# Kernel tuning notes

Measured on AMD Instinct MI355X. Metric: run time of the kernel, lower is better.

## Reference

```python
import jax, jax.numpy as jnp
import numpy as np

P = 16; D = 1024; NH = 16; MAG = 4
B = 2; V = 4; H = 256; W = 512
DEPTH = 6; NE = 2; NM = 3   # dense-early, sparse-middle, rest dense-late
L = (H // P) * (W // P)    # 512 tokens
KEEP = L // 4              # keep_ratio = 0.25 -> 128 hard tokens
HD = D // NH
SCALE = HD ** -0.5


def setup_inputs() -> dict:
    key = jax.random.key(0)
    ks = iter(jax.random.split(key, 64))
    def rn(shape, s=0.02):
        return jax.random.normal(next(ks), shape, jnp.float32) * s
    inp = {}
    inp['x'] = jax.random.normal(next(ks), (B, V, H, W), jnp.float32)
    # select_hard_tokens: per-row randperm(L)[:K], sorted -> deterministic input
    rng = np.random.default_rng(0)
    hi = np.stack([np.sort(rng.permutation(L)[:KEEP]) for _ in range(B)]).astype(np.int32)
    inp['hard_idx'] = jnp.asarray(hi)
    inp['patch_w'] = rn((V, P * P, D)); inp['patch_b'] = jnp.zeros((V, D), jnp.float32)
    inp['var_embed'] = rn((V, D)); inp['var_query'] = rn((D,))
    inp['agg_wq'] = rn((D, D)); inp['agg_wk'] = rn((D, D))
    inp['agg_wv'] = rn((D, D)); inp['agg_wo'] = rn((D, D))
    inp['agg_bo'] = jnp.zeros((D,), jnp.float32)
    inp['pos_embed'] = rn((L, D), 1.0)
    inp['ln1_w'] = jnp.ones((DEPTH, D), jnp.float32); inp['ln1_b'] = jnp.zeros((DEPTH, D), jnp.float32)
    inp['qkv_w'] = rn((DEPTH, D, 3 * D)); inp['qkv_b'] = jnp.zeros((DEPTH, 3 * D), jnp.float32)
    inp['aproj_w'] = rn((DEPTH, D, D)); inp['aproj_b'] = jnp.zeros((DEPTH, D), jnp.float32)
    inp['ln2_w'] = jnp.ones((DEPTH, D), jnp.float32); inp['ln2_b'] = jnp.zeros((DEPTH, D), jnp.float32)
    inp['fc1_w'] = rn((DEPTH, D, 4 * D)); inp['fc1_b'] = jnp.zeros((DEPTH, 4 * D), jnp.float32)
    inp['fc2_w'] = rn((DEPTH, 4 * D, D)); inp['fc2_b'] = jnp.zeros((DEPTH, D), jnp.float32)
    inp['norm_w'] = jnp.ones((D,), jnp.float32); inp['norm_b'] = jnp.zeros((D,), jnp.float32)
    inp['head_w'] = rn((2, D, D)); inp['head_b'] = jnp.zeros((2, D), jnp.float32)
    inp['head_out_w'] = rn((D, (MAG * P) ** 2)); inp['head_out_b'] = jnp.zeros(((MAG * P) ** 2,), jnp.float32)
    inp['p2c1_w'] = rn((4 * MAG * MAG, V, 3, 3)); inp['p2c1_b'] = jnp.zeros((4 * MAG * MAG,), jnp.float32)
    inp['p2c2_w'] = rn((1, 4, 3, 3)); inp['p2c2_b'] = jnp.zeros((1,), jnp.float32)
    inp['cout_w'] = rn((1, 1, 3, 3)); inp['cout_b'] = jnp.zeros((1,), jnp.float32)
    return inp


def _ln(x, g, b):
    m = jnp.mean(x, -1, keepdims=True)
    v = jnp.mean((x - m) ** 2, -1, keepdims=True)
    return (x - m) * jax.lax.rsqrt(v + 1e-5) * g + b


def _conv3x3(x, w, b):
    y = jax.lax.conv_general_dilated(x, w, (1, 1), 'SAME',
                                     dimension_numbers=('NCHW', 'OIHW', 'NCHW'))
    return y + b[None, :, None, None]


def _pixel_shuffle(x, r):
    b, c, h, w = x.shape
    c2 = c // (r * r)
    return x.reshape(b, c2, r, r, h, w).transpose(0, 1, 4, 2, 5, 3).reshape(b, c2, h * r, w * r)


def _block_step(c, p):
    l1w, l1b, qw, qb, pw, pb, l2w, l2b, f1w, f1b, f2w, f2b = p
    bsz, n, _ = c.shape
    hn = _ln(c, l1w, l1b)
    qkv = (hn @ qw + qb).reshape(bsz, n, 3, NH, HD).transpose(2, 0, 3, 1, 4)  # 3,b,h,n,d
    qh, kh, vh = qkv[0], qkv[1], qkv[2]
    att = jax.nn.softmax(jnp.einsum('bhqd,bhkd->bhqk', qh, kh) * SCALE, axis=-1)
    o = jnp.einsum('bhqk,bhkd->bhqd', att, vh).transpose(0, 2, 1, 3).reshape(bsz, n, D)
    c = c + o @ pw + pb
    hn2 = _ln(c, l2w, l2b)
    c = c + jax.nn.gelu(hn2 @ f1w + f1b, approximate=False) @ f2w + f2b
    return c, None


def reference(x, hard_idx, patch_w, patch_b, var_embed, var_query,
              agg_wq, agg_wk, agg_wv, agg_wo, agg_bo, pos_embed,
              ln1_w, ln1_b, qkv_w, qkv_b, aproj_w, aproj_b,
              ln2_w, ln2_b, fc1_w, fc1_b, fc2_w, fc2_b,
              norm_w, norm_b, head_w, head_b, head_out_w, head_out_b,
              p2c1_w, p2c1_b, p2c2_w, p2c2_b, cout_w, cout_b):
    b_, v_, h_img, w_img = x.shape
    hh, ww = h_img // P, w_img // P
    ltok = hh * ww
    # per-variable patch embedding (PatchEmbed with in_chans=1)
    xp = x.reshape(b_, v_, hh, P, ww, P).transpose(0, 1, 2, 4, 3, 5).reshape(b_, v_, ltok, P * P)
    tok = jnp.einsum('bvle,ved->bvld', xp, patch_w) + patch_b[None, :, None, :]
    tok = tok + var_embed[None, :, None, :]
    # aggregate_variables: cross-attention query over V per token
    xf = tok.transpose(0, 2, 1, 3).reshape(b_ * ltok, v_, D)
    q = (var_query @ agg_wq).reshape(NH, HD)
    k = (xf @ agg_wk).reshape(-1, v_, NH, HD)
    vv = (xf @ agg_wv).reshape(-1, v_, NH, HD)
    a = jax.nn.softmax(jnp.einsum('hd,nvhd->nhv', q, k) * SCALE, axis=-1)
    agg = jnp.einsum('nhv,nvhd->nhd', a, vv).reshape(-1, D) @ agg_wo + agg_bo
    xt = agg.reshape(b_, ltok, D) + pos_embed[None]
    stacked = (ln1_w, ln1_b, qkv_w, qkv_b, aproj_w, aproj_b,
               ln2_w, ln2_b, fc1_w, fc1_b, fc2_w, fc2_b)
    def run(c, s, e):
        c, _ = jax.lax.scan(_block_step, c, tuple(ar[s:e] for ar in stacked))
        return c
    # dense early blocks (all tokens)
    xt = run(xt, 0, NE)
    # gather hard tokens -> sparse middle blocks; easy tokens skip via identity
    hard = jnp.take_along_axis(xt, hard_idx[:, :, None].astype(jnp.int32), axis=1)
    hard = run(hard, NE, NE + NM)
    brow = jnp.arange(b_)[:, None]
    xt = xt.at[brow, hard_idx].set(hard)  # merge_tokens (easy = identity)
    # dense late blocks
    xt = run(xt, NE + NM, DEPTH)
    xt = _ln(xt, norm_w, norm_b)
    # decoder head
    for i in range(head_w.shape[0]):
        xt = jax.nn.gelu(xt @ head_w[i] + head_b[i], approximate=False)
    pred = xt @ head_out_w + head_out_b  # (B, L, (MAG*P)^2)
    # unpatchify with scaling=MAG
    h2, w2 = h_img * MAG // P, w_img * MAG // P
    y = pred.reshape(b_, h2, w2, P, P, 1)
    y = jnp.einsum('nhwpqc->nchpwq', y).reshape(b_, 1, h2 * P, w2 * P)
    # residual path2 on raw input channels (out_var_index = all 4 channels here)
    r = jax.nn.gelu(_conv3x3(x, p2c1_w, p2c1_b), approximate=False)
    r = _pixel_shuffle(r, MAG)
    r = _conv3x3(r, p2c2_w, p2c2_b)
    return _conv3x3(y + r, cout_w, cout_b)
```

## Files before the change

kernel.cpp:

```cpp
#include <hip/hip_runtime.h>
#include <math.h>


#define UNIT 1048576L

typedef __attribute__((ext_vector_type(8))) short short8;
typedef __attribute__((ext_vector_type(4))) float f32x4;

#define GLDS(gp, lp) __builtin_amdgcn_global_load_lds( \
    (const __attribute__((address_space(1))) void*)(gp), \
    (__attribute__((address_space(3))) void*)(lp), 16, 0, 0)

__device__ __forceinline__ float gelu_f(float v){
  return 0.5f*v*(1.0f + erff(v*0.70710678118654752440f));
}

__device__ __forceinline__ unsigned short f2bf(float f){
  union { float f; unsigned u; } a; a.f = f;
  unsigned r = a.u + 0x7fffu + ((a.u >> 16) & 1u);
  return (unsigned short)(r >> 16);
}
__device__ __forceinline__ float bf2f(unsigned short u){
  union { unsigned u; float f; } a; a.u = (unsigned)u << 16;
  return a.f;
}

struct WJobs {
  const float* W[4];
  unsigned short* T[4];
  int K[4], N[4];
  int start[4];
};

__global__ __launch_bounds__(256)
void wtrans_multi(WJobs J)
{
  __shared__ float tile[32][33];
  int bx = blockIdx.x;
  int j = 0;
  #pragma unroll
  for (int i = 1; i < 4; ++i) if (bx >= J.start[i]) j = i;
  int local = bx - J.start[j];
  int K = J.K[j], N = J.N[j];
  int nx = N >> 5, tpb = (K >> 5) * nx;
  int bz = local / tpb, rem = local % tpb;
  int k0 = (rem / nx) * 32, n0 = (rem % nx) * 32;
  const float* Wp = J.W[j] + (long)bz * K * N;
  unsigned short* Wo = J.T[j] + (long)bz * K * N;
  int tx = threadIdx.x & 31, ty = threadIdx.x >> 5;
  #pragma unroll
  for (int i = 0; i < 4; ++i)
    tile[ty*4+i][tx] = Wp[(long)(k0 + ty*4 + i)*N + n0 + tx];
  __syncthreads();
  #pragma unroll
  for (int i = 0; i < 4; ++i){
    int n = ty*4 + i;
    Wo[(long)(n0 + n)*K + k0 + tx] = f2bf(tile[tx][n]);
  }
}

template<int TM>
__global__ __launch_bounds__(256)
void gemm_bt(const unsigned short* __restrict__ A, const unsigned short* __restrict__ Wt,
             const float* __restrict__ bias, const float* __restrict__ res,
// ... 81 lines not shown
  #pragma unroll
  for (int i = 0; i < 4; ++i){
    int rbase = row0 + wm + i*16 + kg*4;
    #pragma unroll
    for (int j = 0; j < NJ; ++j){
      int c = col0 + wn + j*16 + ln;
      float bv = bptr ? bptr[c] : 0.f;
      #pragma unroll
      for (int rr2 = 0; rr2 < 4; ++rr2){
        int rrow = rbase + rr2;
        float v = acc[i][j][rr2] + bv;
        if (rptr) v += rptr[(long)rrow*ldc + c];
        if (act == 1) v = gelu_f(v);
        if (Cf) Cf[(long)rrow*ldc + c] = v;
        if (Cb) Cb[(long)rrow*ldc + c] = f2bf(v);
      }
    }
  }
}

__global__ __launch_bounds__(256)
void reduce_ep(const float* __restrict__ Cp, int splits, int nbat, long MN, int N,
               const float* __restrict__ bias, const float* __restrict__ res, long sRes,
               float* __restrict__ Cf, unsigned short* __restrict__ Cb, long sC, int act)
{
  long e4 = (long)blockIdx.x*256 + threadIdx.x;
  if (e4 >= (long)nbat*MN/4) return;
  long e = e4 * 4;
  int b = (int)(e / MN); long r = e % MN; int col = (int)(r % N);
  float4 s = *(const float4*)&Cp[(long)b*MN + r];
  for (int sp = 1; sp < splits; ++sp){
    float4 p = *(const float4*)&Cp[((long)sp*nbat + b)*MN + r];
    s.x += p.x; s.y += p.y; s.z += p.z; s.w += p.w;
  }
  if (bias){
    float4 bv = *(const float4*)&bias[col];
    s.x += bv.x; s.y += bv.y; s.z += bv.z; s.w += bv.w;
  }
  if (res){
    float4 rv = *(const float4*)&res[(long)b*sRes + r];
    s.x += rv.x; s.y += rv.y; s.z += rv.z; s.w += rv.w;
  }
  if (act == 1){
    s.x = gelu_f(s.x); s.y = gelu_f(s.y); s.z = gelu_f(s.z); s.w = gelu_f(s.w);
  }
  if (Cf) *(float4*)&Cf[(long)b*sC + r] = s;
  if (Cb){
    unsigned q0 = (unsigned)f2bf(s.x) | ((unsigned)f2bf(s.y) << 16);
    unsigned q1 = (unsigned)f2bf(s.z) | ((unsigned)f2bf(s.w) << 16);
    uint2 pk = {q0, q1};
    *(uint2*)&Cb[(long)b*sC + r] = pk;
  }
}

__global__ __launch_bounds__(256)
void ln_bf(const float* __restrict__ x, const float* __restrict__ g,
           const float* __restrict__ b, unsigned short* __restrict__ y)
{
  long r = blockIdx.x;
  int t = threadIdx.x;
  float4 v = ((const float4*)(x + r*1024))[t];
  float s  = v.x + v.y + v.z + v.w;
  float ss = v.x*v.x + v.y*v.y + v.z*v.z + v.w*v.w;
  #pragma unroll
  for (int o = 32; o; o >>= 1){ s += __shfl_xor(s, o); ss += __shfl_xor(ss, o); }
  __shared__ float sa[4], sb[4];
  int w = t >> 6, lane = t & 63;
  if (!lane){ sa[w] = s; sb[w] = ss; }
  __syncthreads();
  s  = sa[0] + sa[1] + sa[2] + sa[3];
  ss = sb[0] + sb[1] + sb[2] + sb[3];
  float mean = s * (1.0f/1024.0f);
  float var  = ss * (1.0f/1024.0f) - mean*mean;
  float rstd = rsqrtf(var + 1e-5f);
  float4 gv = ((const float4*)g)[t];
  float4 bv = ((const float4*)b)[t];
  float ox = (v.x-mean)*rstd*gv.x + bv.x;
  float oy = (v.y-mean)*rstd*gv.y + bv.y;
  float oz = (v.z-mean)*rstd*gv.z + bv.z;
  float ow = (v.w-mean)*rstd*gv.w + bv.w;
  unsigned q0 = (unsigned)f2bf(ox) | ((unsigned)f2bf(oy) << 16);
  unsigned q1 = (unsigned)f2bf(oz) | ((unsigned)f2bf(ow) << 16);
  uint2 pk = {q0, q1};
  *(uint2*)&y[r*1024 + t*4] = pk;
}

__global__ void xp_extract(const float* __restrict__ x, unsigned short* __restrict__ xp)
{
  int idx = blockIdx.x * 256 + threadIdx.x;
  int e4 = idx & 63;
  int lt = (idx >> 6) & 511;
  int zz = idx >> 15;
  int e  = e4 << 2;
  int py = e >> 4, px0 = e & 15;
  int hy = lt >> 5, wx = lt & 31;
  float4 v = *(const float4*)&x[((long)zz*256 + hy*16 + py)*512 + wx*16 + px0];
  unsigned q0 = (unsigned)f2bf(v.x) | ((unsigned)f2bf(v.y) << 16);
  unsigned q1 = (unsigned)f2bf(v.z) | ((unsigned)f2bf(v.w) << 16);
  uint2 pk = {q0, q1};
  ((uint2*)xp)[idx] = pk;
}

__global__ void pb2_combine(const float* __restrict__ pb, const float* __restrict__ ve,
                            float* __restrict__ out)
{
  int i = blockIdx.x * 256 + threadIdx.x;
  out[i] = pb[i] + ve[i];
}

__global__ void qproj(const float* __restrict__ vq, const float* __restrict__ wq,
                      float* __restrict__ q)
{
  int n = blockIdx.x * 64 + threadIdx.x;
  float s = 0.f;
  for (int k = 0; k < 1024; ++k) s += vq[k] * wq[(long)k*1024 + n];
  q[n] = s;
}

__global__ void wk_fold(const float* __restrict__ wk, const float* __restrict__ qv,
                        float* __restrict__ wt)
{
  int i = blockIdx.x * 256 + threadIdx.x;
  int h = i & 15, D = i >> 4;
  const float* wr = wk + (long)D*1024 + h*64;
  const float* qr = qv + h*64;
  float s = 0.f;
  #pragma unroll
  for (int d = 0; d < 64; ++d) s += wr[d]*qr[d];
  wt[h*1024 + D] = s;
}

__global__ __launch_bounds__(64)
void agg_attn2(const unsigned short* __restrict__ tok, const float* __restrict__ vb,
               const float* __restrict__ wt, unsigned short* __restrict__ out)
{
  int l = blockIdx.x, h = blockIdx.y, b = blockIdx.z, t = threadIdx.x;
  const float* wh = wt + h*1024;
  float sc[4];
  #pragma unroll
  for (int v = 0; v < 4; ++v){
    const unsigned short* tr = tok + ((((long)b*4 + v)*512 + l) << 10);
    float s = 0.f;
    #pragma unroll
    for (int j = 0; j < 16; ++j){
      int D = t + j*64;
      s += bf2f(tr[D]) * wh[D];
    }
    #pragma unroll
    for (int o = 32; o; o >>= 1) s += __shfl_xor(s, o);
    sc[v] = s * 0.125f;
  }
  float m = fmaxf(fmaxf(sc[0], sc[1]), fmaxf(sc[2], sc[3]));
  float e0 = __expf(sc[0]-m), e1 = __expf(sc[1]-m), e2 = __expf(sc[2]-m), e3 = __expf(sc[3]-m);
  float inv = 1.0f / (e0 + e1 + e2 + e3);
  long base = (((long)b*4)*512 + l)*1024 + h*64 + t;
  float o = e0*vb[base] + e1*vb[base + 512*1024] + e2*vb[base + 2*512*1024] + e3*vb[base + 3*512*1024];
  out[(((long)b*512 + l) << 10) + h*64 + t] = f2bf(o * inv);
}

__global__ __launch_bounds__(256)
void attn_mfma(const float* __restrict__ qkv, unsigned short* __restrict__ out, int N)
{
  int h = blockIdx.y, b = blockIdx.z;
  int row0 = blockIdx.x * 32;
  int t = threadIdx.x;
  int wave = t >> 6, lane = t & 63;
  int ln = lane & 15, kg = lane >> 4;
  int mtile = wave & 1, khalf = wave >> 1;
  const float* base = qkv + (long)b * N * 3072;

  __shared__ __align__(16) unsigned short Ks[128*72];
  __shared__ __align__(16) unsigned short Vt[64*136];
  __shared__ __align__(16) unsigned short Pw[4][16*72];
  __shared__ float Obuf[4][16][68];
  __shared__ float Mbuf[4][16], Lbuf[4][16];

  short8 qf[2];
  {
    const float* qp = base + (long)(row0 + mtile*16 + ln)*3072 + h*64;
    #pragma unroll
    for (int s = 0; s < 2; ++s){
      float4 a = *(const float4*)(qp + s*32 + kg*8);
      float4 c = *(const float4*)(qp + s*32 + kg*8 + 4);
      short8 q;
      q[0] = (short)f2bf(a.x*0.125f); q[1] = (short)f2bf(a.y*0.125f);
      q[2] = (short)f2bf(a.z*0.125f); q[3] = (short)f2bf(a.w*0.125f);
      q[4] = (short)f2bf(c.x*0.125f); q[5] = (short)f2bf(c.y*0.125f);
      q[6] = (short)f2bf(c.z*0.125f); q[7] = (short)f2bf(c.w*0.125f);
      qf[s] = q;
    }
  }

  f32x4 z = {0.f, 0.f, 0.f, 0.f};
  f32x4 O[4] = {z, z, z, z};
  float mrow[4] = {-1e30f, -1e30f, -1e30f, -1e30f};
  float lrow[4] = {0.f, 0.f, 0.f, 0.f};
  unsigned short* pw = &Pw[wave][0];

  for (int j0 = 0; j0 < N; j0 += 128){
    #pragma unroll
    for (int it = 0; it < 2; ++it){
      int key = (t >> 2) + it*64;
      int dg = (t & 3) * 16;
      const float* kp = base + (long)(j0 + key)*3072 + 1024 + h*64 + dg;
      float4 k0 = *(const float4*)kp,     k1 = *(const float4*)(kp+4);
      float4 k2 = *(const float4*)(kp+8), k3 = *(const float4*)(kp+12);
      unsigned short* kd = &Ks[key*72 + dg];
      uint2 p0 = { (unsigned)f2bf(k0.x) | ((unsigned)f2bf(k0.y)<<16),
                   (unsigned)f2bf(k0.z) | ((unsigned)f2bf(k0.w)<<16) };
      uint2 p1 = { (unsigned)f2bf(k1.x) | ((unsigned)f2bf(k1.y)<<16),
                   (unsigned)f2bf(k1.z) | ((unsigned)f2bf(k1.w)<<16) };
      uint2 p2 = { (unsigned)f2bf(k2.x) | ((unsigned)f2bf(k2.y)<<16),
                   (unsigned)f2bf(k2.z) | ((unsigned)f2bf(k2.w)<<16) };
      uint2 p3 = { (unsigned)f2bf(k3.x) | ((unsigned)f2bf(k3.y)<<16),
                   (unsigned)f2bf(k3.z) | ((unsigned)f2bf(k3.w)<<16) };
      *(uint2*)&kd[0]  = p0; *(uint2*)&kd[4]  = p1;
      *(uint2*)&kd[8]  = p2; *(uint2*)&kd[12] = p3;
      const float* vp = base + (long)(j0 + key)*3072 + 2048 + h*64 + dg;
      float4 v0 = *(const float4*)vp,     v1 = *(const float4*)(vp+4);
      float4 v2 = *(const float4*)(vp+8), v3 = *(const float4*)(vp+12);
      float vv[16];
      vv[0]=v0.x; vv[1]=v0.y; vv[2]=v0.z; vv[3]=v0.w;
      vv[4]=v1.x; vv[5]=v1.y; vv[6]=v1.z; vv[7]=v1.w;
      vv[8]=v2.x; vv[9]=v2.y; vv[10]=v2.z; vv[11]=v2.w;
      vv[12]=v3.x; vv[13]=v3.y; vv[14]=v3.z; vv[15]=v3.w;
      #pragma unroll
      for (int i = 0; i < 16; ++i) Vt[(dg+i)*136 + key] = f2bf(vv[i]);
    }
    __syncthreads();

    f32x4 acc[4] = {z, z, z, z};
    const unsigned short* kbase = &Ks[(khalf*64)*72];
    #pragma unroll
    for (int s = 0; s < 2; ++s){
      #pragma unroll
      for (int nt = 0; nt < 4; ++nt){
        short8 bf = *(const short8*)&kbase[(nt*16 + ln)*72 + s*32 + kg*8];
        acc[nt] = __builtin_amdgcn_mfma_f32_16x16x32_bf16(qf[s], bf, acc[nt], 0, 0, 0);
      }
    }

    #pragma unroll
    for (int r = 0; r < 4; ++r){
      float mt = fmaxf(fmaxf(acc[0][r], acc[1][r]), fmaxf(acc[2][r], acc[3][r]));
      #pragma unroll
      for (int o = 1; o < 16; o <<= 1) mt = fmaxf(mt, __shfl_xor(mt, o));
      float m_new = fmaxf(mrow[r], mt);
      float alpha = __expf(mrow[r] - m_new);
      float ps = 0.f;
      #pragma unroll
// ... 39 lines not shown
  float ma = Mbuf[wa][lr],  mb2 = Mbuf[wa+2][lr];
  float la = Lbuf[wa][lr],  lb  = Lbuf[wa+2][lr];
  float mm = fmaxf(ma, mb2);
  float ea = __expf(ma - mm), eb = __expf(mb2 - mm);
  float linv = 1.0f / (la*ea + lb*eb);
  ea *= linv; eb *= linv;
  float4 a0 = *(const float4*)&Obuf[wa][lr][d0];
  float4 a1 = *(const float4*)&Obuf[wa][lr][d0+4];
  float4 b0 = *(const float4*)&Obuf[wa+2][lr][d0];
  float4 b1 = *(const float4*)&Obuf[wa+2][lr][d0+4];
  float o0 = a0.x*ea + b0.x*eb, o1 = a0.y*ea + b0.y*eb;
  float o2 = a0.z*ea + b0.z*eb, o3 = a0.w*ea + b0.w*eb;
  float o4 = a1.x*ea + b1.x*eb, o5 = a1.y*ea + b1.y*eb;
  float o6 = a1.z*ea + b1.z*eb, o7 = a1.w*ea + b1.w*eb;
  unsigned q0 = (unsigned)f2bf(o0) | ((unsigned)f2bf(o1) << 16);
  unsigned q1 = (unsigned)f2bf(o2) | ((unsigned)f2bf(o3) << 16);
  unsigned q2 = (unsigned)f2bf(o4) | ((unsigned)f2bf(o5) << 16);
  unsigned q3 = (unsigned)f2bf(o6) | ((unsigned)f2bf(o7) << 16);
  uint4 pk = {q0, q1, q2, q3};
  *(uint4*)&out[((long)(b*N + row0 + row))*1024 + h*64 + d0] = pk;
}

__global__ __launch_bounds__(256)
void gather_rows(const float* __restrict__ src, const int* __restrict__ idx,
                 float* __restrict__ dst)
{
  int r = blockIdx.x;
  int b = r >> 7, i = r & 127;
  int s = idx[b*128 + i];
  ((float4*)(dst + (long)r*1024))[threadIdx.x] =
      ((const float4*)(src + ((long)b*512 + s)*1024))[threadIdx.x];
}
__global__ __launch_bounds__(256)
void scatter_rows(const float* __restrict__ src, const int* __restrict__ idx,
                  float* __restrict__ dst)
{
  int r = blockIdx.x;
  int b = r >> 7, i = r & 127;
  int s = idx[b*128 + i];
  ((float4*)(dst + ((long)b*512 + s)*1024))[threadIdx.x] =
      ((const float4*)(src + (long)r*1024))[threadIdx.x];
}

__global__ __launch_bounds__(256)
void conv1_v4(const float* __restrict__ x, const float* __restrict__ w,
              const float* __restrict__ bi, unsigned short* __restrict__ out)
{
  __shared__ unsigned short obuf[256*68];
  int t = threadIdx.x;
  int id = blockIdx.x*256 + t;
  int px = id & 511, py = (id >> 9) & 255, bb = id >> 17;
  float in[4][9];
  #pragma unroll
  for (int ci = 0; ci < 4; ++ci){
    const float* xc = x + ((long)(bb*4 + ci)*256)*512;
    #pragma unroll
    for (int ky = 0; ky < 3; ++ky){
      int yy = py + ky - 1;
      #pragma unroll
      for (int kx = 0; kx < 3; ++kx){
        int xx = px + kx - 1;
        bool ok = ((unsigned)yy < 256u) && ((unsigned)xx < 512u);
        in[ci][ky*3+kx] = ok ? xc[yy*512 + xx] : 0.f;
      }
    }
  }
  unsigned short* orow = &obuf[t*68];
// ... 120 lines not shown
  }
}

static inline void gemm_go(hipStream_t st, int TM, const unsigned short* A,
                           const unsigned short* Wt,
                           const float* bias, const float* res, float* Cf, unsigned short* Cb,
                           float* Cp, int splits,
                           int M, int N, int K, int batches,
                           long sA, long sW, long sBias, long sRes, long sC,
                           int wmod, int act)
{
  dim3 g(N/128, M/TM, batches*splits);
  long MN = (long)M*N;
  if (TM == 128)
    gemm_bt<128><<<g, 256, 0, st>>>(A, Wt, bias, res, Cf, Cb, Cp, MN, splits,
                                    M, N, K, N, sA, sW, sBias, sRes, sC, wmod, act);
  else
    gemm_bt<64><<<g, 256, 0, st>>>(A, Wt, bias, res, Cf, Cb, Cp, MN, splits,
                                   M, N, K, N, sA, sW, sBias, sRes, sC, wmod, act);
}

static inline void reduce_go(hipStream_t st, const float* Cp, int splits, int nbat,
                             long MN, int N, const float* bias, const float* res, long sRes,
                             float* Cf, unsigned short* Cb, long sC, int act)
{
  long total4 = (long)nbat*MN/4;
  reduce_ep<<<(int)((total4 + 255)/256), 256, 0, st>>>(Cp, splits, nbat, MN, N,
                                                       bias, res, sRes, Cf, Cb, sC, act);
}

static inline void wmulti_go(hipStream_t st, int njobs,
                             const float* W0, unsigned short* T0, int K0, int N0, int nb0,
                             const float* W1, unsigned short* T1, int K1, int N1, int nb1,
                             const float* W2, unsigned short* T2, int K2, int N2, int nb2,
                             const float* W3, unsigned short* T3, int K3, int N3, int nb3)
{
  WJobs J;
  const float* Ws[4] = {W0, W1, W2, W3};
  unsigned short* Ts[4] = {T0, T1, T2, T3};
  int Ks[4] = {K0, K1, K2, K3}, Ns[4] = {N0, N1, N2, N3}, nbs[4] = {nb0, nb1, nb2, nb3};
  int acc = 0;
  for (int i = 0; i < 4; ++i){
    if (i < njobs){
      J.W[i] = Ws[i]; J.T[i] = Ts[i]; J.K[i] = Ks[i]; J.N[i] = Ns[i];
      J.start[i] = acc;
      acc += nbs[i] * (Ks[i] >> 5) * (Ns[i] >> 5);
    } else {
      J.W[i] = Ws[0]; J.T[i] = Ts[0]; J.K[i] = 32; J.N[i] = 32;
      J.start[i] = 0x7fffffff;
    }
  }
  wtrans_multi<<<acc, 256, 0, st>>>(J);
}

extern "C" void kernel_launch(void* const* d_in, const int* in_sizes, int n_in,
                              void* d_out, int out_size, void* d_ws, size_t ws_size,
                              hipStream_t stream)
{
  const float* x         = (const float*)d_in[0];
  const int*   hard_idx  = (const int*)  d_in[1];
  const float* patch_w   = (const float*)d_in[2];
  const float* patch_b   = (const float*)d_in[3];
  const float* var_embed = (const float*)d_in[4];
  const float* var_query = (const float*)d_in[5];
  const float* agg_wq    = (const float*)d_in[6];
  const float* agg_wk    = (const float*)d_in[7];
  const float* agg_wv    = (const float*)d_in[8];
  const float* agg_wo    = (const float*)d_in[9];
  const float* agg_bo    = (const float*)d_in[10];
  const float* pos_embed = (const float*)d_in[11];
  const float* ln1_w     = (const float*)d_in[12];
  const float* ln1_b     = (const float*)d_in[13];
  const float* qkv_w     = (const float*)d_in[14];
  const float* qkv_b     = (const float*)d_in[15];
  const float* aproj_w   = (const float*)d_in[16];
  const float* aproj_b   = (const float*)d_in[17];
  const float* ln2_w     = (const float*)d_in[18];
  const float* ln2_b     = (const float*)d_in[19];
  const float* fc1_w     = (const float*)d_in[20];
  const float* fc1_b     = (const float*)d_in[21];
  const float* fc2_w     = (const float*)d_in[22];
  const float* fc2_b     = (const float*)d_in[23];
  const float* norm_w    = (const float*)d_in[24];
  const float* norm_b    = (const float*)d_in[25];
  const float* head_w    = (const float*)d_in[26];
  const float* head_b    = (const float*)d_in[27];
  const float* head_out_w= (const float*)d_in[28];
  const float* head_out_b= (const float*)d_in[29];
  const float* p2c1_w    = (const float*)d_in[30];
  const float* p2c1_b    = (const float*)d_in[31];
  const float* p2c2_w    = (const float*)d_in[32];
  const float* p2c2_b    = (const float*)d_in[33];
  const float* cout_w    = (const float*)d_in[34];
  const float* cout_b    = (const float*)d_in[35];

  float* ws = (float*)d_ws;
  float* xt   = ws;
  float* r2   = ws + 1*UNIT;
  float* qkvb = ws + 5*UNIT;
  float* pred = ws + 8*UNIT;
  unsigned short* rbig = (unsigned short*)(ws + 8*UNIT);
  float* vb   = ws + 12*UNIT;
  float* Cp   = ws + 12*UNIT;
  unsigned short* b16 = (unsigned short*)(ws + 16*UNIT);
  unsigned short* hn_bf    = b16;
  unsigned short* ao_bf    = b16 + 1*UNIT;
  unsigned short* ff_bf    = b16 + 2*UNIT;
  unsigned short* xp_bf    = b16 + 6*UNIT;
  unsigned short* tok_bf   = b16 + 7*UNIT;
  unsigned short* aggin_bf = b16 + 11*UNIT;
  unsigned short* wt_a     = b16 + 12*UNIT;
  float* tail = ws + 28*UNIT;
  float* pb2  = tail;
  float* qv   = tail + 4096;
  float* wtl  = tail + 5120;
  float* hbuf = tail + 21504;

  conv1_v4<<<1024, 256, 0, stream>>>(x, p2c1_w, p2c1_b, rbig);
  conv2_v3<<<dim3(32, 64, 2), 256, 0, stream>>>(rbig, p2c2_w, p2c2_b, r2);

  unsigned short* wt_patch = wt_a;
  unsigned short* wt_wv    = wt_a + 1*UNIT;
  unsigned short* wt_wo    = wt_a + 2*UNIT;
  pb2_combine<<<16, 256, 0, stream>>>(patch_b, var_embed, pb2);
  xp_extract<<<1024, 256, 0, stream>>>(x, xp_bf);
  qproj<<<16, 64, 0, stream>>>(var_query, agg_wq, qv);
  wk_fold<<<64, 256, 0, stream>>>(agg_wk, qv, wtl);
  wmulti_go(stream, 3,
            patch_w, wt_patch, 256, 1024, 4,
            agg_wv,  wt_wv,   1024, 1024, 1,
            agg_wo,  wt_wo,   1024, 1024, 1,
            nullptr, nullptr, 0, 0, 0);
  gemm_go(stream, 128, xp_bf, wt_patch, pb2, nullptr, nullptr, tok_bf, nullptr, 1,
          512, 1024, 256, 8, 512L*256, 256L*1024, 1024, 0, 512L*1024, 4, 0);
  gemm_go(stream, 128, tok_bf, wt_wv, nullptr, nullptr, vb, nullptr, nullptr, 1,
          512, 1024, 1024, 8, 512L*1024, 0, 0, 0, 512L*1024, 1, 0);
  agg_attn2<<<dim3(512, 16, 2), 64, 0, stream>>>(tok_bf, vb, wtl, aggin_bf);
  gemm_go(stream, 64, aggin_bf, wt_wo, nullptr, nullptr, nullptr, nullptr, Cp, 2,
          512, 1024, 1024, 2, 512L*1024, 0, 0, 0, 512L*1024, 1, 0);
  reduce_go(stream, Cp, 2, 2, 512L*1024, 1024, agg_bo, pos_embed, 0, xt, nullptr,
            512L*1024, 0);

  unsigned short* wt_qkv   = wt_a;
  unsigned short* wt_aproj = wt_a + 3*UNIT;
  unsigned short* wt_fc1   = wt_a + 4*UNIT;
  unsigned short* wt_fc2   = wt_a + 8*UNIT;

  auto run_block = [&](float* cur, int Nt, int d){
    int rows = 2 * Nt;
    bool dense = (rows >= 1024);
    int TMbig = dense ? 128 : 64;
    long MNq = (long)rows*3072, MNa = (long)rows*1024, MNf = (long)rows*4096;
    wmulti_go(stream, 4,
              qkv_w   + (long)d*1024*3072, wt_qkv,   1024, 3072, 1,
              aproj_w + (long)d*1024*1024, wt_aproj, 1024, 1024, 1,
              fc1_w   + (long)d*1024*4096, wt_fc1,   1024, 4096, 1,
              fc2_w   + (long)d*4096*1024, wt_fc2,   4096, 1024, 1);
    ln_bf<<<rows, 256, 0, stream>>>(cur, ln1_w + d*1024, ln1_b + d*1024, hn_bf);
    gemm_go(stream, TMbig, hn_bf, wt_qkv, qkv_b + d*3072, nullptr, qkvb, nullptr, nullptr, 1,
            rows, 3072, 1024, 1, 0, 0, 0, 0, 0, 1, 0);
    attn_mfma<<<dim3(Nt/32, 16, 2), 256, 0, stream>>>(qkvb, ao_bf, Nt);
    {
      int sk = dense ? 4 : 8;
      gemm_go(stream, TMbig, ao_bf, wt_aproj, nullptr, nullptr, nullptr, nullptr, Cp, sk,
              rows, 1024, 1024, 1, 0, 0, 0, 0, 0, 1, 0);
      reduce_go(stream, Cp, sk, 1, MNa, 1024, aproj_b + d*1024, cur, MNa, cur, nullptr, MNa, 0);
    }
    ln_bf<<<rows, 256, 0, stream>>>(cur, ln2_w + d*1024, ln2_b + d*1024, hn_bf);
    if (dense){
      gemm_go(stream, 128, hn_bf, wt_fc1, fc1_b + d*4096, nullptr, nullptr, ff_bf, nullptr, 1,
              rows, 4096, 1024, 1, 0, 0, 0, 0, 0, 1, 1);
    } else {
      gemm_go(stream, 64, hn_bf, wt_fc1, nullptr, nullptr, nullptr, nullptr, Cp, 2,
              rows, 4096, 1024, 1, 0, 0, 0, 0, 0, 1, 1);
      reduce_go(stream, Cp, 2, 1, MNf, 4096, fc1_b + d*4096, nullptr, 0, nullptr, ff_bf, MNf, 1);
    }
    {
      int sk = dense ? 4 : 8;
      gemm_go(stream, TMbig, ff_bf, wt_fc2, nullptr, nullptr, nullptr, nullptr, Cp, sk,
              rows, 1024, 4096, 1, 0, 0, 0, 0, 0, 1, 0);
      reduce_go(stream, Cp, sk, 1, MNa, 1024, fc2_b + d*1024, cur, MNa, cur, nullptr, MNa, 0);
    }
  };

  run_block(xt, 512, 0);
  run_block(xt, 512, 1);
  gather_rows<<<256, 256, 0, stream>>>(xt, hard_idx, hbuf);
  run_block(hbuf, 128, 2);
  run_block(hbuf, 128, 3);
  run_block(hbuf, 128, 4);
  scatter_rows<<<256, 256, 0, stream>>>(hbuf, hard_idx, xt);
  run_block(xt, 512, 5);

  unsigned short* wt_h1 = wt_a;
  unsigned short* wt_h2 = wt_a + 1*UNIT;
  unsigned short* wt_ho = wt_a + 2*UNIT;
  wmulti_go(stream, 3,
            head_w,              wt_h1, 1024, 1024, 1,
            head_w + 1024L*1024, wt_h2, 1024, 1024, 1,
            head_out_w,          wt_ho, 1024, 4096, 1,
            nullptr, nullptr, 0, 0, 0);
  ln_bf<<<1024, 256, 0, stream>>>(xt, norm_w, norm_b, hn_bf);
  gemm_go(stream, 64, hn_bf, wt_h1, nullptr, nullptr, nullptr, nullptr, Cp, 2,
          1024, 1024, 1024, 1, 0, 0, 0, 0, 0, 1, 1);
  reduce_go(stream, Cp, 2, 1, 1024L*1024, 1024, head_b, nullptr, 0, nullptr, ao_bf,
            1024L*1024, 1);
  gemm_go(stream, 64, ao_bf, wt_h2, nullptr, nullptr, nullptr, nullptr, Cp, 2,
          1024, 1024, 1024, 1, 0, 0, 0, 0, 0, 1, 1);
  reduce_go(stream, Cp, 2, 1, 1024L*1024, 1024, head_b + 1024, nullptr, 0, nullptr, hn_bf,
            1024L*1024, 1);
  gemm_go(stream, 128, hn_bf, wt_ho, head_out_b, nullptr, pred, nullptr, nullptr, 1,
          1024, 4096, 1024, 1, 0, 0, 0, 0, 0, 1, 0);

  cout_fused<<<dim3(32, 64, 2), 256, 0, stream>>>(pred, r2, cout_w, cout_b, (float*)d_out);
}
```

Baseline: 1.373 ms.

## Fuse residual reduce with LayerNorm, batch weight transposes, keep QKV in bf16

All weight transposes for every layer and the head now run in one upfront launch instead of one launch per block. The split-K reduce is fused with the next LayerNorm (reduce_ln), the gather is fused with LN, and the scatter is folded into the last sparse block's reduce epilogue via an index table. The QKV output and the aggregation V are stored as bf16, so the attention kernels read half the bytes and skip conversion. The QKV GEMM now uses split-K plus a reduce, which adds a partial-buffer round trip. The workspace footprint grows to hold all transposed weights.

```diff
diff --git a/kernel.cpp b/kernel.cpp
--- a/kernel.cpp
+++ b/kernel.cpp
@@ -26,10 +26,10 @@
 }
 
 struct WJobs {
-  const float* W[4];
-  unsigned short* T[4];
-  int K[4], N[4];
-  int start[4];
+  const float* W[10];
+  unsigned short* T[10];
+  int K[10], N[10];
+  int start[10];
 };
 
 __global__ __launch_bounds__(256)
@@ -39,7 +39,7 @@
   int bx = blockIdx.x;
   int j = 0;
   #pragma unroll
-  for (int i = 1; i < 4; ++i) if (bx >= J.start[i]) j = i;
+  for (int i = 1; i < 10; ++i) if (bx >= J.start[i]) j = i;
   int local = bx - J.start[j];
   int K = J.K[j], N = J.N[j];
   int nx = N >> 5, tpb = (K >> 5) * nx;
@@ -167,7 +167,8 @@
 __global__ __launch_bounds__(256)
 void reduce_ep(const float* __restrict__ Cp, int splits, int nbat, long MN, int N,
                const float* __restrict__ bias, const float* __restrict__ res, long sRes,
-               float* __restrict__ Cf, unsigned short* __restrict__ Cb, long sC, int act)
+               float* __restrict__ Cf, unsigned short* __restrict__ Cb, long sC, int act,
+               const int* __restrict__ sidx)
 {
   long e4 = (long)blockIdx.x*256 + threadIdx.x;
   if (e4 >= (long)nbat*MN/4) return;
@@ -189,13 +190,70 @@
   if (act == 1){
     s.x = gelu_f(s.x); s.y = gelu_f(s.y); s.z = gelu_f(s.z); s.w = gelu_f(s.w);
   }
-  if (Cf) *(float4*)&Cf[(long)b*sC + r] = s;
+  if (Cf){
+    if (sidx){
+      int rw = (int)(r >> 10); int bt = rw >> 7, ii = rw & 127;
+      long orow = (long)bt*512 + sidx[bt*128 + ii];
+      *(float4*)&Cf[orow*1024 + (r & 1023)] = s;
+    } else {
+      *(float4*)&Cf[(long)b*sC + r] = s;
+    }
+  }
   if (Cb){
     unsigned q0 = (unsigned)f2bf(s.x) | ((unsigned)f2bf(s.y) << 16);
     unsigned q1 = (unsigned)f2bf(s.z) | ((unsigned)f2bf(s.w) << 16);
     uint2 pk = {q0, q1};
     *(uint2*)&Cb[(long)b*sC + r] = pk;
   }
+}
+
+__global__ __launch_bounds__(256)
+void reduce_ln(const float* __restrict__ Cp, int splits, int nbat, long MN,
+               const float* __restrict__ bias,
+               const float* __restrict__ res, long sRes,
+               float* __restrict__ cur,
+               const float* __restrict__ g, const float* __restrict__ b,
+               unsigned short* __restrict__ hn)
+{
+  int row = blockIdx.x;
+  int t = threadIdx.x;
+  int rpb = (int)(MN >> 10);
+  int bb = row / rpb;
+  long r = (long)(row - bb*rpb)*1024 + t*4;
+  float4 s = *(const float4*)&Cp[(long)bb*MN + r];
+  for (int sp = 1; sp < splits; ++sp){
+    float4 p = *(const float4*)&Cp[((long)sp*nbat + bb)*MN + r];
+    s.x += p.x; s.y += p.y; s.z += p.z; s.w += p.w;
+  }
+  int col = t*4;
+  float4 bv = *(const float4*)&bias[col];
+  s.x += bv.x; s.y += bv.y; s.z += bv.z; s.w += bv.w;
+  float4 rv = *(const float4*)&res[(long)bb*sRes + r];
+  s.x += rv.x; s.y += rv.y; s.z += rv.z; s.w += rv.w;
+  *(float4*)&cur[(long)row*1024 + col] = s;
+  float sm = s.x + s.y + s.z + s.w;
+  float ss = s.x*s.x + s.y*s.y + s.z*s.z + s.w*s.w;
+  #pragma unroll
+  for (int o = 32; o; o >>= 1){ sm += __shfl_xor(sm, o); ss += __shfl_xor(ss, o); }
+  __shared__ float sa[4], sb[4];
+  int w = t >> 6, lane = t & 63;
+  if (!lane){ sa[w] = sm; sb[w] = ss; }
+  __syncthreads();
+  sm = sa[0] + sa[1] + sa[2] + sa[3];
+  ss = sb[0] + sb[1] + sb[2] + sb[3];
+  float mean = sm * (1.0f/1024.0f);
+  float var  = ss * (1.0f/1024.0f) - mean*mean;
+  float rstd = rsqrtf(var + 1e-5f);
+  float4 gv = ((const float4*)g)[t];
+  float4 bv2 = ((const float4*)b)[t];
+  float ox = (s.x-mean)*rstd*gv.x + bv2.x;
+  float oy = (s.y-mean)*rstd*gv.y + bv2.y;
+  float oz = (s.z-mean)*rstd*gv.z + bv2.z;
+  float ow = (s.w-mean)*rstd*gv.w + bv2.w;
+  unsigned q0 = (unsigned)f2bf(ox) | ((unsigned)f2bf(oy) << 16);
+  unsigned q1 = (unsigned)f2bf(oz) | ((unsigned)f2bf(ow) << 16);
+  uint2 pk = {q0, q1};
+  *(uint2*)&hn[(long)row*1024 + col] = pk;
 }
 
 __global__ __launch_bounds__(256)
@@ -230,6 +288,41 @@
   *(uint2*)&y[r*1024 + t*4] = pk;
 }
 
+__global__ __launch_bounds__(256)
+void gather_ln(const float* __restrict__ src, const int* __restrict__ idx,
+               float* __restrict__ dst, const float* __restrict__ g,
+               const float* __restrict__ b, unsigned short* __restrict__ hn)
+{
+  int r = blockIdx.x, t = threadIdx.x;
+  int bb = r >> 7, i = r & 127;
+  int s0 = idx[bb*128 + i];
+  float4 v = ((const float4*)(src + ((long)bb*512 + s0)*1024))[t];
+  ((float4*)(dst + (long)r*1024))[t] = v;
+  float s  = v.x + v.y + v.z + v.w;
+  float ss = v.x*v.x + v.y*v.y + v.z*v.z + v.w*v.w;
+  #pragma unroll
+  for (int o = 32; o; o >>= 1){ s += __shfl_xor(s, o); ss += __shfl_xor(ss, o); }
+  __shared__ float sa[4], sb[4];
+  int w = t >> 6, lane = t & 63;
+  if (!lane){ sa[w] = s; sb[w] = ss; }
+  __syncthreads();
+  s  = sa[0] + sa[1] + sa[2] + sa[3];
+  ss = sb[0] + sb[1] + sb[2] + sb[3];
+  float mean = s * (1.0f/1024.0f);
+  float var  = ss * (1.0f/1024.0f) - mean*mean;
+  float rstd = rsqrtf(var + 1e-5f);
+  float4 gv = ((const float4*)g)[t];
+  float4 bv = ((const float4*)b)[t];
+  float ox = (v.x-mean)*rstd*gv.x + bv.x;
+  float oy = (v.y-mean)*rstd*gv.y + bv.y;
+  float oz = (v.z-mean)*rstd*gv.z + bv.z;
+  float ow = (v.w-mean)*rstd*gv.w + bv.w;
+  unsigned q0 = (unsigned)f2bf(ox) | ((unsigned)f2bf(oy) << 16);
+  unsigned q1 = (unsigned)f2bf(oz) | ((unsigned)f2bf(ow) << 16);
+  uint2 pk = {q0, q1};
+  *(uint2*)&hn[(long)r*1024 + t*4] = pk;
+}
+
 __global__ void xp_extract(const float* __restrict__ x, unsigned short* __restrict__ xp)
 {
   int idx = blockIdx.x * 256 + threadIdx.x;
@@ -276,7 +369,7 @@
 }
 
 __global__ __launch_bounds__(64)
-void agg_attn2(const unsigned short* __restrict__ tok, const float* __restrict__ vb,
+void agg_attn2(const unsigned short* __restrict__ tok, const unsigned short* __restrict__ vb,
                const float* __restrict__ wt, unsigned short* __restrict__ out)
 {
   int l = blockIdx.x, h = blockIdx.y, b = blockIdx.z, t = threadIdx.x;
@@ -299,12 +392,14 @@
   float e0 = __expf(sc[0]-m), e1 = __expf(sc[1]-m), e2 = __expf(sc[2]-m), e3 = __expf(sc[3]-m);
   float inv = 1.0f / (e0 + e1 + e2 + e3);
   long base = (((long)b*4)*512 + l)*1024 + h*64 + t;
-  float o = e0*vb[base] + e1*vb[base + 512*1024] + e2*vb[base + 2*512*1024] + e3*vb[base + 3*512*1024];
+  float o = e0*bf2f(vb[base]) + e1*bf2f(vb[base + 512*1024])
+          + e2*bf2f(vb[base + 2*512*1024]) + e3*bf2f(vb[base + 3*512*1024]);
   out[(((long)b*512 + l) << 10) + h*64 + t] = f2bf(o * inv);
 }
 
 __global__ __launch_bounds__(256)
-void attn_mfma(const float* __restrict__ qkv, unsigned short* __restrict__ out, int N)
+void attn_mfma(const unsigned short* __restrict__ qkv, unsigned short* __restrict__ out,
+               int N)
 {
   int h = blockIdx.y, b = blockIdx.z;
   int row0 = blockIdx.x * 32;
@@ -312,7 +407,7 @@
   int wave = t >> 6, lane = t & 63;
   int ln = lane & 15, kg = lane >> 4;
   int mtile = wave & 1, khalf = wave >> 1;
-  const float* base = qkv + (long)b * N * 3072;
+  const unsigned short* base = qkv + (long)b * N * 3072;
 
   __shared__ __align__(16) unsigned short Ks[128*72];
   __shared__ __align__(16) unsigned short Vt[64*136];
@@ -322,16 +417,17 @@
 
   short8 qf[2];
   {
-    const float* qp = base + (long)(row0 + mtile*16 + ln)*3072 + h*64;
+    const unsigned short* qp = base + (long)(row0 + mtile*16 + ln)*3072 + h*64;
     #pragma unroll
     for (int s = 0; s < 2; ++s){
-      float4 a = *(const float4*)(qp + s*32 + kg*8);
-      float4 c = *(const float4*)(qp + s*32 + kg*8 + 4);
+      uint4 qa = *(const uint4*)(qp + s*32 + kg*8);
+      unsigned qs[4] = {qa.x, qa.y, qa.z, qa.w};
       short8 q;
-      q[0] = (short)f2bf(a.x*0.125f); q[1] = (short)f2bf(a.y*0.125f);
-      q[2] = (short)f2bf(a.z*0.125f); q[3] = (short)f2bf(a.w*0.125f);
-      q[4] = (short)f2bf(c.x*0.125f); q[5] = (short)f2bf(c.y*0.125f);
-      q[6] = (short)f2bf(c.z*0.125f); q[7] = (short)f2bf(c.w*0.125f);
+      #pragma unroll
+      for (int i = 0; i < 4; ++i){
+        q[2*i]   = (short)f2bf(bf2f((unsigned short)(qs[i] & 0xffff)) * 0.125f);
+        q[2*i+1] = (short)f2bf(bf2f((unsigned short)(qs[i] >> 16)) * 0.125f);
+      }
       qf[s] = q;
     }
   }
@@ -347,30 +443,26 @@
     for (int it = 0; it < 2; ++it){
       int key = (t >> 2) + it*64;
       int dg = (t & 3) * 16;
-      const float* kp = base + (long)(j0 + key)*3072 + 1024 + h*64 + dg;
-      float4 k0 = *(const float4*)kp,     k1 = *(const float4*)(kp+4);
-      float4 k2 = *(const float4*)(kp+8), k3 = *(const float4*)(kp+12);
+      const unsigned short* kp = base + (long)(j0 + key)*3072 + 1024 + h*64 + dg;
+      uint4 ka = *(const uint4*)kp;
+      uint4 kb = *(const uint4*)(kp + 8);
       unsigned short* kd = &Ks[key*72 + dg];
-      uint2 p0 = { (unsigned)f2bf(k0.x) | ((unsigned)f2bf(k0.y)<<16),
-                   (unsigned)f2bf(k0.z) | ((unsigned)f2bf(k0.w)<<16) };
-      uint2 p1 = { (unsigned)f2bf(k1.x) | ((unsigned)f2bf(k1.y)<<16),
-                   (unsigned)f2bf(k1.z) | ((unsigned)f2bf(k1.w)<<16) };
-      uint2 p2 = { (unsigned)f2bf(k2.x) | ((unsigned)f2bf(k2.y)<<16),
-                   (unsigned)f2bf(k2.z) | ((unsigned)f2bf(k2.w)<<16) };
-      uint2 p3 = { (unsigned)f2bf(k3.x) | ((unsigned)f2bf(k3.y)<<16),
-                   (unsigned)f2bf(k3.z) | ((unsigned)f2bf(k3.w)<<16) };
-      *(uint2*)&kd[0]  = p0; *(uint2*)&kd[4]  = p1;
-      *(uint2*)&kd[8]  = p2; *(uint2*)&kd[12] = p3;
-      const float* vp = base + (long)(j0 + key)*3072 + 2048 + h*64 + dg;
-      float4 v0 = *(const float4*)vp,     v1 = *(const float4*)(vp+4);
-      float4 v2 = *(const float4*)(vp+8), v3 = *(const float4*)(vp+12);
-      float vv[16];
-      vv[0]=v0.x; vv[1]=v0.y; vv[2]=v0.z; vv[3]=v0.w;
-      vv[4]=v1.x; vv[5]=v1.y; vv[6]=v1.z; vv[7]=v1.w;
-      vv[8]=v2.x; vv[9]=v2.y; vv[10]=v2.z; vv[11]=v2.w;
-      vv[12]=v3.x; vv[13]=v3.y; vv[14]=v3.z; vv[15]=v3.w;
-      #pragma unroll
-      for (int i = 0; i < 16; ++i) Vt[(dg+i)*136 + key] = f2bf(vv[i]);
+      *(uint4*)&kd[0] = ka;
+      *(uint4*)&kd[8] = kb;
+      const unsigned short* vp = base + (long)(j0 + key)*3072 + 2048 + h*64 + dg;
+      uint4 va = *(const uint4*)vp;
+      uint4 vb4 = *(const uint4*)(vp + 8);
+      unsigned short vv[16];
+      vv[0]=(unsigned short)(va.x&0xffff);  vv[1]=(unsigned short)(va.x>>16);
+      vv[2]=(unsigned short)(va.y&0xffff);  vv[3]=(unsigned short)(va.y>>16);
+      vv[4]=(unsigned short)(va.z&0xffff);  vv[5]=(unsigned short)(va.z>>16);
+      vv[6]=(unsigned short)(va.w&0xffff);  vv[7]=(unsigned short)(va.w>>16);
+      vv[8]=(unsigned short)(vb4.x&0xffff); vv[9]=(unsigned short)(vb4.x>>16);
+      vv[10]=(unsigned short)(vb4.y&0xffff); vv[11]=(unsigned short)(vb4.y>>16);
+      vv[12]=(unsigned short)(vb4.z&0xffff); vv[13]=(unsigned short)(vb4.z>>16);
+      vv[14]=(unsigned short)(vb4.w&0xffff); vv[15]=(unsigned short)(vb4.w>>16);
+      #pragma unroll
+      for (int i = 0; i < 16; ++i) Vt[(dg+i)*136 + key] = vv[i];
     }
     __syncthreads();
 
@@ -456,27 +548,6 @@
 }
 
 __global__ __launch_bounds__(256)
-void gather_rows(const float* __restrict__ src, const int* __restrict__ idx,
-                 float* __restrict__ dst)
-{
-  int r = blockIdx.x;
-  int b = r >> 7, i = r & 127;
-  int s = idx[b*128 + i];
-  ((float4*)(dst + (long)r*1024))[threadIdx.x] =
-      ((const float4*)(src + ((long)b*512 + s)*1024))[threadIdx.x];
-}
-__global__ __launch_bounds__(256)
-void scatter_rows(const float* __restrict__ src, const int* __restrict__ idx,
-                  float* __restrict__ dst)
-{
-  int r = blockIdx.x;
-  int b = r >> 7, i = r & 127;
-  int s = idx[b*128 + i];
-  ((float4*)(dst + ((long)b*512 + s)*1024))[threadIdx.x] =
-      ((const float4*)(src + (long)r*1024))[threadIdx.x];
-}
-
-__global__ __launch_bounds__(256)
 void conv1_v4(const float* __restrict__ x, const float* __restrict__ w,
               const float* __restrict__ bi, unsigned short* __restrict__ out)
 {
@@ -643,35 +714,13 @@
 
 static inline void reduce_go(hipStream_t st, const float* Cp, int splits, int nbat,
                              long MN, int N, const float* bias, const float* res, long sRes,
-                             float* Cf, unsigned short* Cb, long sC, int act)
+                             float* Cf, unsigned short* Cb, long sC, int act,
+                             const int* sidx)
 {
   long total4 = (long)nbat*MN/4;
   reduce_ep<<<(int)((total4 + 255)/256), 256, 0, st>>>(Cp, splits, nbat, MN, N,
-                                                       bias, res, sRes, Cf, Cb, sC, act);
-}
-
-static inline void wmulti_go(hipStream_t st, int njobs,
-                             const float* W0, unsigned short* T0, int K0, int N0, int nb0,
-                             const float* W1, unsigned short* T1, int K1, int N1, int nb1,
-                             const float* W2, unsigned short* T2, int K2, int N2, int nb2,
-                             const float* W3, unsigned short* T3, int K3, int N3, int nb3)
-{
-  WJobs J;
-  const float* Ws[4] = {W0, W1, W2, W3};
-  unsigned short* Ts[4] = {T0, T1, T2, T3};
-  int Ks[4] = {K0, K1, K2, K3}, Ns[4] = {N0, N1, N2, N3}, nbs[4] = {nb0, nb1, nb2, nb3};
-  int acc = 0;
-  for (int i = 0; i < 4; ++i){
-    if (i < njobs){
-      J.W[i] = Ws[i]; J.T[i] = Ts[i]; J.K[i] = Ks[i]; J.N[i] = Ns[i];
-      J.start[i] = acc;
-      acc += nbs[i] * (Ks[i] >> 5) * (Ns[i] >> 5);
-    } else {
-      J.W[i] = Ws[0]; J.T[i] = Ts[0]; J.K[i] = 32; J.N[i] = 32;
-      J.start[i] = 0x7fffffff;
-    }
-  }
-  wtrans_multi<<<acc, 256, 0, st>>>(J);
+                                                       bias, res, sRes, Cf, Cb, sC, act,
+                                                       sidx);
 }
 
 extern "C" void kernel_launch(void* const* d_in, const int* in_sizes, int n_in,
@@ -718,11 +767,8 @@
   float* ws = (float*)d_ws;
   float* xt   = ws;
   float* r2   = ws + 1*UNIT;
-  float* qkvb = ws + 5*UNIT;
   float* pred = ws + 8*UNIT;
   unsigned short* rbig = (unsigned short*)(ws + 8*UNIT);
-  float* vb   = ws + 12*UNIT;
-  float* Cp   = ws + 12*UNIT;
   unsigned short* b16 = (unsigned short*)(ws + 16*UNIT);
   unsigned short* hn_bf    = b16;
   unsigned short* ao_bf    = b16 + 1*UNIT;
@@ -730,106 +776,118 @@
   unsigned short* xp_bf    = b16 + 6*UNIT;
   unsigned short* tok_bf   = b16 + 7*UNIT;
   unsigned short* aggin_bf = b16 + 11*UNIT;
-  unsigned short* wt_a     = b16 + 12*UNIT;
+  unsigned short* qkvb_bf  = b16 + 12*UNIT;
+  unsigned short* vb_bf    = b16 + 15*UNIT;
   float* tail = ws + 28*UNIT;
   float* pb2  = tail;
   float* qv   = tail + 4096;
   float* wtl  = tail + 5120;
   float* hbuf = tail + 21504;
+  unsigned short* wt_all   = (unsigned short*)(ws + 40*UNIT);
+  unsigned short* wt_patch = wt_all;
+  unsigned short* wt_wv    = wt_all + 1*UNIT;
+  unsigned short* wt_wo    = wt_all + 2*UNIT;
+  unsigned short* wt_h1    = wt_all + 3*UNIT;
+  unsigned short* wt_h2    = wt_all + 4*UNIT;
+  unsigned short* wt_ho    = wt_all + 5*UNIT;
+  unsigned short* wt_qkv   = wt_all + 9*UNIT;
+  unsigned short* wt_aproj = wt_all + 27*UNIT;
+  unsigned short* wt_fc1   = wt_all + 33*UNIT;
+  unsigned short* wt_fc2   = wt_all + 57*UNIT;
+  float* Cp = ws + 84*UNIT;
 
   conv1_v4<<<1024, 256, 0, stream>>>(x, p2c1_w, p2c1_b, rbig);
   conv2_v3<<<dim3(32, 64, 2), 256, 0, stream>>>(rbig, p2c2_w, p2c2_b, r2);
 
-  unsigned short* wt_patch = wt_a;
-  unsigned short* wt_wv    = wt_a + 1*UNIT;
-  unsigned short* wt_wo    = wt_a + 2*UNIT;
+  {
+    WJobs J;
+    const float* Ws[10] = {patch_w, agg_wv, agg_wo, head_w, head_w + 1024L*1024,
+                           head_out_w, qkv_w, aproj_w, fc1_w, fc2_w};
+    unsigned short* Ts[10] = {wt_patch, wt_wv, wt_wo, wt_h1, wt_h2,
+                              wt_ho, wt_qkv, wt_aproj, wt_fc1, wt_fc2};
+    int Ks[10]  = {256, 1024, 1024, 1024, 1024, 1024, 1024, 1024, 1024, 4096};
+    int Ns[10]  = {1024,1024, 1024, 1024, 1024, 4096, 3072, 1024, 4096, 1024};
+    int nbs[10] = {4, 1, 1, 1, 1, 1, 6, 6, 6, 6};
+    int acc = 0;
+    for (int i = 0; i < 10; ++i){
+      J.W[i] = Ws[i]; J.T[i] = Ts[i]; J.K[i] = Ks[i]; J.N[i] = Ns[i];
+      J.start[i] = acc;
+      acc += nbs[i] * (Ks[i] >> 5) * (Ns[i] >> 5);
+    }
+    wtrans_multi<<<acc, 256, 0, stream>>>(J);
+  }
+
   pb2_combine<<<16, 256, 0, stream>>>(patch_b, var_embed, pb2);
   xp_extract<<<1024, 256, 0, stream>>>(x, xp_bf);
   qproj<<<16, 64, 0, stream>>>(var_query, agg_wq, qv);
   wk_fold<<<64, 256, 0, stream>>>(agg_wk, qv, wtl);
-  wmulti_go(stream, 3,
-            patch_w, wt_patch, 256, 1024, 4,
-            agg_wv,  wt_wv,   1024, 1024, 1,
-            agg_wo,  wt_wo,   1024, 1024, 1,
-            nullptr, nullptr, 0, 0, 0);
   gemm_go(stream, 128, xp_bf, wt_patch, pb2, nullptr, nullptr, tok_bf, nullptr, 1,
           512, 1024, 256, 8, 512L*256, 256L*1024, 1024, 0, 512L*1024, 4, 0);
-  gemm_go(stream, 128, tok_bf, wt_wv, nullptr, nullptr, vb, nullptr, nullptr, 1,
+  gemm_go(stream, 128, tok_bf, wt_wv, nullptr, nullptr, nullptr, vb_bf, nullptr, 1,
           512, 1024, 1024, 8, 512L*1024, 0, 0, 0, 512L*1024, 1, 0);
-  agg_attn2<<<dim3(512, 16, 2), 64, 0, stream>>>(tok_bf, vb, wtl, aggin_bf);
+  agg_attn2<<<dim3(512, 16, 2), 64, 0, stream>>>(tok_bf, vb_bf, wtl, aggin_bf);
   gemm_go(stream, 64, aggin_bf, wt_wo, nullptr, nullptr, nullptr, nullptr, Cp, 2,
-          512, 1024, 1024, 2, 512L*1024, 0, 0, 0, 512L*1024, 1, 0);
-  reduce_go(stream, Cp, 2, 2, 512L*1024, 1024, agg_bo, pos_embed, 0, xt, nullptr,
-            512L*1024, 0);
-
-  unsigned short* wt_qkv   = wt_a;
-  unsigned short* wt_aproj = wt_a + 3*UNIT;
-  unsigned short* wt_fc1   = wt_a + 4*UNIT;
-  unsigned short* wt_fc2   = wt_a + 8*UNIT;
-
-  auto run_block = [&](float* cur, int Nt, int d){
+          512, 1024, 1024, 2, 512L*1024, 0, 0, 0, 0, 1, 0);
+  reduce_ln<<<1024, 256, 0, stream>>>(Cp, 2, 2, 512L*1024, agg_bo, pos_embed, 0,
+                                      xt, ln1_w, ln1_b, hn_bf);
+
+  auto run_block = [&](float* cur, int Nt, int d, const float* nw, const float* nbp,
+                       int fc2mode){
     int rows = 2 * Nt;
     bool dense = (rows >= 1024);
     int TMbig = dense ? 128 : 64;
-    long MNq = (long)rows*3072, MNa = (long)rows*1024, MNf = (long)rows*4096;
-    wmulti_go(stream, 4,
-              qkv_w   + (long)d*1024*3072, wt_qkv,   1024, 3072, 1,
-              aproj_w + (long)d*1024*1024, wt_aproj, 1024, 1024, 1,
-              fc1_w   + (long)d*1024*4096, wt_fc1,   1024, 4096, 1,
-              fc2_w   + (long)d*4096*1024, wt_fc2,   4096, 1024, 1);
-    ln_bf<<<rows, 256, 0, stream>>>(cur, ln1_w + d*1024, ln1_b + d*1024, hn_bf);
-    gemm_go(stream, TMbig, hn_bf, wt_qkv, qkv_b + d*3072, nullptr, qkvb, nullptr, nullptr, 1,
-            rows, 3072, 1024, 1, 0, 0, 0, 0, 0, 1, 0);
-    attn_mfma<<<dim3(Nt/32, 16, 2), 256, 0, stream>>>(qkvb, ao_bf, Nt);
-    {
-      int sk = dense ? 4 : 8;
-      gemm_go(stream, TMbig, ao_bf, wt_aproj, nullptr, nullptr, nullptr, nullptr, Cp, sk,
-              rows, 1024, 1024, 1, 0, 0, 0, 0, 0, 1, 0);
-      reduce_go(stream, Cp, sk, 1, MNa, 1024, aproj_b + d*1024, cur, MNa, cur, nullptr, MNa, 0);
-    }
-    ln_bf<<<rows, 256, 0, stream>>>(cur, ln2_w + d*1024, ln2_b + d*1024, hn_bf);
+    long MNa = (long)rows*1024, MNf = (long)rows*4096;
+    int qsk = dense ? 2 : 4;
+    gemm_go(stream, TMbig, hn_bf, wt_qkv + (long)d*3*UNIT, nullptr, nullptr, nullptr,
+            nullptr, Cp, qsk, rows, 3072, 1024, 1, 0, 0, 0, 0, 0, 1, 0);
+    reduce_go(stream, Cp, qsk, 1, (long)rows*3072, 3072, qkv_b + d*3072, nullptr, 0,
+              nullptr, qkvb_bf, 0, 0, nullptr);
+    attn_mfma<<<dim3(Nt/32, 16, 2), 256, 0, stream>>>(qkvb_bf, ao_bf, Nt);
+    int sk = dense ? 4 : 8;
+    gemm_go(stream, TMbig, ao_bf, wt_aproj + (long)d*UNIT, nullptr, nullptr, nullptr,
+            nullptr, Cp, sk, rows, 1024, 1024, 1, 0, 0, 0, 0, 0, 1, 0);
+    reduce_ln<<<rows, 256, 0, stream>>>(Cp, sk, 1, MNa, aproj_b + d*1024, cur, 0,
+                                        cur, ln2_w + d*1024, ln2_b + d*1024, hn_bf);
     if (dense){
-      gemm_go(stream, 128, hn_bf, wt_fc1, fc1_b + d*4096, nullptr, nullptr, ff_bf, nullptr, 1,
-              rows, 4096, 1024, 1, 0, 0, 0, 0, 0, 1, 1);
+      gemm_go(stream, 128, hn_bf, wt_fc1 + (long)d*4*UNIT, fc1_b + d*4096, nullptr,
+              nullptr, ff_bf, nullptr, 1, rows, 4096, 1024, 1, 0, 0, 0, 0, 0, 1, 1);
     } else {
-      gemm_go(stream, 64, hn_bf, wt_fc1, nullptr, nullptr, nullptr, nullptr, Cp, 2,
-              rows, 4096, 1024, 1, 0, 0, 0, 0, 0, 1, 1);
-      reduce_go(stream, Cp, 2, 1, MNf, 4096, fc1_b + d*4096, nullptr, 0, nullptr, ff_bf, MNf, 1);
-    }
-    {
-      int sk = dense ? 4 : 8;
-      gemm_go(stream, TMbig, ff_bf, wt_fc2, nullptr, nullptr, nullptr, nullptr, Cp, sk,
-              rows, 1024, 4096, 1, 0, 0, 0, 0, 0, 1, 0);
-      reduce_go(stream, Cp, sk, 1, MNa, 1024, fc2_b + d*1024, cur, MNa, cur, nullptr, MNa, 0);
-    }
+      gemm_go(stream, 64, hn_bf, wt_fc1 + (long)d*4*UNIT, nullptr, nullptr, nullptr,
+              nullptr, Cp, 2, rows, 4096, 1024, 1, 0, 0, 0, 0, 0, 1, 1);
+      reduce_go(stream, Cp, 2, 1, MNf, 4096, fc1_b + d*4096, nullptr, 0,
+                nullptr, ff_bf, 0, 1, nullptr);
+    }
+    gemm_go(stream, TMbig, ff_bf, wt_fc2 + (long)d*4*UNIT, nullptr, nullptr, nullptr,
+            nullptr, Cp, sk, rows, 1024, 4096, 1, 0, 0, 0, 0, 0, 1, 0);
+    if (fc2mode == 0)
+      reduce_ln<<<rows, 256, 0, stream>>>(Cp, sk, 1, MNa, fc2_b + d*1024, cur, 0,
+                                          cur, nw, nbp, hn_bf);
+    else if (fc2mode == 1)
+      reduce_go(stream, Cp, sk, 1, MNa, 1024, fc2_b + d*1024, cur, 0,
+                cur, nullptr, 0, 0, nullptr);
+    else
+      reduce_go(stream, Cp, sk, 1, MNa, 1024, fc2_b + d*1024, hbuf, 0,
+                xt, nullptr, 0, 0, hard_idx);
   };
 
-  run_block(xt, 512, 0);
-  run_block(xt, 512, 1);
-  gather_rows<<<256, 256, 0, stream>>>(xt, hard_idx, hbuf);
-  run_block(hbuf, 128, 2);
-  run_block(hbuf, 128, 3);
-  run_block(hbuf, 128, 4);
-  scatter_rows<<<256, 256, 0, stream>>>(hbuf, hard_idx, xt);
-  run_block(xt, 512, 5);
-
-  unsigned short* wt_h1 = wt_a;
-  unsigned short* wt_h2 = wt_a + 1*UNIT;
-  unsigned short* wt_ho = wt_a + 2*UNIT;
-  wmulti_go(stream, 3,
-            head_w,              wt_h1, 1024, 1024, 1,
-            head_w + 1024L*1024, wt_h2, 1024, 1024, 1,
-            head_out_w,          wt_ho, 1024, 4096, 1,
-            nullptr, nullptr, 0, 0, 0);
-  ln_bf<<<1024, 256, 0, stream>>>(xt, norm_w, norm_b, hn_bf);
+  run_block(xt, 512, 0, ln1_w + 1024, ln1_b + 1024, 0);
+  run_block(xt, 512, 1, nullptr, nullptr, 1);
+  gather_ln<<<256, 256, 0, stream>>>(xt, hard_idx, hbuf,
+                                     ln1_w + 2*1024, ln1_b + 2*1024, hn_bf);
+  run_block(hbuf, 128, 2, ln1_w + 3*1024, ln1_b + 3*1024, 0);
+  run_block(hbuf, 128, 3, ln1_w + 4*1024, ln1_b + 4*1024, 0);
+  run_block(hbuf, 128, 4, nullptr, nullptr, 2);
+  ln_bf<<<1024, 256, 0, stream>>>(xt, ln1_w + 5*1024, ln1_b + 5*1024, hn_bf);
+  run_block(xt, 512, 5, norm_w, norm_b, 0);
+
   gemm_go(stream, 64, hn_bf, wt_h1, nullptr, nullptr, nullptr, nullptr, Cp, 2,
           1024, 1024, 1024, 1, 0, 0, 0, 0, 0, 1, 1);
-  reduce_go(stream, Cp, 2, 1, 1024L*1024, 1024, head_b, nullptr, 0, nullptr, ao_bf,
-            1024L*1024, 1);
+  reduce_go(stream, Cp, 2, 1, 1024L*1024, 1024, head_b, nullptr, 0,
+            nullptr, ao_bf, 0, 1, nullptr);
   gemm_go(stream, 64, ao_bf, wt_h2, nullptr, nullptr, nullptr, nullptr, Cp, 2,
           1024, 1024, 1024, 1, 0, 0, 0, 0, 0, 1, 1);
-  reduce_go(stream, Cp, 2, 1, 1024L*1024, 1024, head_b + 1024, nullptr, 0, nullptr, hn_bf,
-            1024L*1024, 1);
+  reduce_go(stream, Cp, 2, 1, 1024L*1024, 1024, head_b + 1024, nullptr, 0,
+            nullptr, hn_bf, 0, 1, nullptr);
   gemm_go(stream, 128, hn_bf, wt_ho, head_out_b, nullptr, pred, nullptr, nullptr, 1,
           1024, 4096, 1024, 1, 0, 0, 0, 0, 0, 1, 0);
 
```

Measured after the change: 1.339 ms. 1.03x faster.
